# Performance work log

Measured on AMD Instinct MI355X. Metric: run time of the kernel, lower is better.

Reference implementation:

```python
import jax, jax.numpy as jnp
import numpy as np

EPS = 1e-5
TOP_K = 2


def setup_inputs() -> dict:
    key = jax.random.key(0)
    ks = jax.random.split(key, 6)
    T, H, F, E = 4096, 1024, 2816, 8
    scale = 0.02
    return {
        "hidden_states": jax.random.normal(ks[0], (T, H), dtype=jnp.float32),
        "ln_w": jnp.ones((H,), dtype=jnp.float32),
        "router_w": jax.random.normal(ks[1], (H, E), dtype=jnp.float32) * scale,
        "w_gate": jax.random.normal(ks[2], (E, H, F), dtype=jnp.float32) * scale,
        "w_up": jax.random.normal(ks[3], (E, H, F), dtype=jnp.float32) * scale,
        "w_down": jax.random.normal(ks[4], (E, F, H), dtype=jnp.float32) * scale,
    }


def reference(hidden_states, ln_w, router_w, w_gate, w_up, w_down):
    # RMSNorm (LlamaRMSNorm)
    var = jnp.mean(hidden_states * hidden_states, axis=-1, keepdims=True)
    x = hidden_states * jax.lax.rsqrt(var + EPS) * ln_w  # [T, H]

    # TopKRouter: softmax over experts, then top-k probs/indices
    logits = x @ router_w                     # [T, E]
    probs = jax.nn.softmax(logits, axis=-1)
    topk_p, topk_i = jax.lax.top_k(probs, TOP_K)  # [T, K]

    # Dense combine weights [T, E]: prob for routed experts, 0 otherwise
    T = x.shape[0]
    combine = jnp.zeros_like(probs).at[jnp.arange(T)[:, None], topk_i].add(topk_p)

    # Experts: Llama-style gated MLP (SwiGLU); loop over fixed small expert set
    out = jnp.zeros_like(x)
    for e in range(w_gate.shape[0]):
        h = jax.nn.silu(x @ w_gate[e]) * (x @ w_up[e])   # [T, F]
        out = out + combine[:, e:e + 1] * (h @ w_down[e])
    return out
```

## Files before the change

### kernel.cpp

```cpp
#include <hip/hip_runtime.h>

#define T_TOK 4096
#define H_DIM 1024
#define F_DIM 2816
#define E_NUM 8
#define EPSV 1e-5f

typedef unsigned short u16;
typedef __attribute__((ext_vector_type(8))) short bf16x8;
typedef __attribute__((ext_vector_type(4))) float f32x4;

__device__ __forceinline__ u16 f2bf(float f) {
  union { float f; unsigned u; } c; c.f = f;
  unsigned u = c.u;
  return (u16)((u + 0x7FFFu + ((u >> 16) & 1u)) >> 16);
}

__device__ __forceinline__ void llds16(const u16* g, u16* l) {
  __builtin_amdgcn_global_load_lds(
      (const __attribute__((address_space(1))) unsigned int*)g,
      (__attribute__((address_space(3))) unsigned int*)l, 16, 0, 0);
}

__global__ __launch_bounds__(256) void router_kernel(
    const float* __restrict__ hs, const float* __restrict__ lnw,
    const float* __restrict__ rw, u16* __restrict__ x_h,
    int* __restrict__ cnt, int* __restrict__ list,
    float* __restrict__ wcomb) {
  const int wave = threadIdx.x >> 6;
  const int lane = threadIdx.x & 63;
  const int t = blockIdx.x * 4 + wave;
  const float* row = hs + (size_t)t * H_DIM;

  float4 v[4];
  float ss = 0.f;
#pragma unroll
  for (int j = 0; j < 4; ++j) {
    v[j] = ((const float4*)row)[j * 64 + lane];
    ss += v[j].x * v[j].x + v[j].y * v[j].y + v[j].z * v[j].z + v[j].w * v[j].w;
  }
#pragma unroll
  for (int m = 32; m; m >>= 1) ss += __shfl_xor(ss, m, 64);
  const float inv = rsqrtf(ss * (1.0f / H_DIM) + EPSV);

  float lg[E_NUM];
#pragma unroll
  for (int e = 0; e < E_NUM; ++e) lg[e] = 0.f;

#pragma unroll
  for (int j = 0; j < 4; ++j) {
    const int idx = j * 64 + lane;
    const int h0 = idx * 4;
    float4 w4 = ((const float4*)lnw)[idx];
    float xv[4] = {v[j].x * inv * w4.x, v[j].y * inv * w4.y,
                   v[j].z * inv * w4.z, v[j].w * inv * w4.w};
    ushort4 xs;
    xs.x = f2bf(xv[0]); xs.y = f2bf(xv[1]); xs.z = f2bf(xv[2]); xs.w = f2bf(xv[3]);
    ((ushort4*)(x_h + (size_t)t * H_DIM))[idx] = xs;
#pragma unroll
    for (int q = 0; q < 4; ++q) {
      const float* rr = rw + (size_t)(h0 + q) * E_NUM;
      float4 a = ((const float4*)rr)[0];
      float4 b = ((const float4*)rr)[1];
      lg[0] += xv[q] * a.x; lg[1] += xv[q] * a.y;
      lg[2] += xv[q] * a.z; lg[3] += xv[q] * a.w;
      lg[4] += xv[q] * b.x; lg[5] += xv[q] * b.y;
      lg[6] += xv[q] * b.z; lg[7] += xv[q] * b.w;
    }
  }
#pragma unroll
  for (int e = 0; e < E_NUM; ++e)
#pragma unroll
    for (int m = 32; m; m >>= 1) lg[e] += __shfl_xor(lg[e], m, 64);

  if (lane == 0) {
    float mx = lg[0];
#pragma unroll
    for (int e = 1; e < E_NUM; ++e) mx = fmaxf(mx, lg[e]);
    float p[E_NUM], s = 0.f;
#pragma unroll
    for (int e = 0; e < E_NUM; ++e) { p[e] = __expf(lg[e] - mx); s += p[e]; }
    const float invs = 1.0f / s;
    int e1 = 0; float b1 = p[0];
#pragma unroll
    for (int e = 1; e < E_NUM; ++e) if (p[e] > b1) { b1 = p[e]; e1 = e; }
    int e2 = -1; float b2 = -1.f;
#pragma unroll
    for (int e = 0; e < E_NUM; ++e) if (e != e1 && p[e] > b2) { b2 = p[e]; e2 = e; }
    b1 *= invs; b2 *= invs;
    int p1 = atomicAdd(&cnt[e1], 1);
    list[e1 * T_TOK + p1] = t; wcomb[e1 * T_TOK + p1] = b1;
    int p2 = atomicAdd(&cnt[e2], 1);
    list[e2 * T_TOK + p2] = t; wcomb[e2 * T_TOK + p2] = b2;
  }
}

__global__ void offsets_kernel(const int* __restrict__ cnt, int* __restrict__ offs) {
  if (threadIdx.x == 0) {
    int s = 0;
    for (int e = 0; e < E_NUM; ++e) { offs[e] = s; s += cnt[e]; }
  }
}

#define TPW 5632
__global__ __launch_bounds__(256) void transpose_cvt_all(
    const float* __restrict__ wg, const float* __restrict__ wu,
    const float* __restrict__ wd, u16* __restrict__ wgT,
    u16* __restrict__ wuT, u16* __restrict__ wdT) {
  __shared__ float tile[128][37];
  const int bx = blockIdx.x;
  const int which = bx / TPW;
  const int rem = bx - which * TPW;
  const int e = rem / 704;
  const int t = rem - e * 704;
  const float* in; u16* outp; int R, C, rt, ct;
  if (which == 0)      { in = wg; outp = wgT; R = H_DIM; C = F_DIM; rt = t / 88; ct = t - rt * 88; }
  else if (which == 1) { in = wu; outp = wuT; R = H_DIM; C = F_DIM; rt = t / 88; ct = t - rt * 88; }
  else                 { in = wd; outp = wdT; R = F_DIM; C = H_DIM; rt = t >> 5; ct = t & 31; }
  const size_t base = (size_t)e * R * C;
  const int r0 = rt * 128, c0 = ct * 32;
  const int tid = threadIdx.x;

  const int rr = tid >> 3, cq = tid & 7;
#pragma unroll
  for (int i = 0; i < 4; ++i) {
    float4 v = *(const float4*)(in + base + (size_t)(r0 + rr + 32 * i) * C + c0 + cq * 4);
    float* dst = &tile[rr + 32 * i][cq * 4];
    dst[0] = v.x; dst[1] = v.y; dst[2] = v.z; dst[3] = v.w;
  }
  __syncthreads();

  const int cc = tid >> 4, rq0 = tid & 15;
#pragma unroll
  for (int jj = 0; jj < 4; ++jj) {
    const int c = cc + 16 * (jj & 1);
    const int rq = rq0 + 16 * (jj >> 1);
    ushort4 o;
    o.x = f2bf(tile[rq * 4 + 0][c]);
    o.y = f2bf(tile[rq * 4 + 1][c]);
    o.z = f2bf(tile[rq * 4 + 2][c]);
    o.w = f2bf(tile[rq * 4 + 3][c]);
    *(ushort4*)(outp + base + (size_t)(c0 + c) * R + r0 + rq * 4) = o;
  }
}

__global__ __launch_bounds__(256) void gemm1_kernel(
    const u16* __restrict__ x_h, const u16* __restrict__ wgT,
    const u16* __restrict__ wuT, const int* __restrict__ cnt,
    const int* __restrict__ offs, const int* __restrict__ list,
    u16* __restrict__ hbuf) {
  const int e = blockIdx.z;
  const int n_e = cnt[e];
  const int rt = blockIdx.y;
  if (rt * 128 >= n_e) return;
  const int ft = blockIdx.x;

  __shared__ __align__(16) u16 As[2][128 * 64];
  __shared__ __align__(16) u16 Bgs[2][64 * 64];
  __shared__ __align__(16) u16 Bus[2][64 * 64];

  const int tid = threadIdx.x;
  const int wv = tid >> 6, lane = tid & 63;
  const int wm = wv >> 1, wn = wv & 1;
  const int lrow = lane & 15, quad = lane >> 4;
  const int srow = lane >> 3, schunk = lane & 7;

  const u16* agp[4];
#pragma unroll
  for (int i = 0; i < 4; ++i) {
    const int rl = wv * 32 + i * 8 + srow;
    int gr = rt * 128 + rl; if (gr >= n_e) gr = n_e - 1;
    const int tkn = list[e * T_TOK + gr];
    agp[i] = x_h + (size_t)tkn * H_DIM + ((schunk ^ (rl & 7)) << 3);
  }
  const size_t wb = ((size_t)e * F_DIM + (size_t)ft * 64) * H_DIM;
  const u16* bgp[2]; const u16* bup[2];
#pragma unroll
  for (int i = 0; i < 2; ++i) {
    const int r = wv * 16 + i * 8 + srow;
    const size_t g = wb + (size_t)r * H_DIM + ((schunk ^ (r & 7)) << 3);
    bgp[i] = wgT + g;
    bup[i] = wuT + g;
  }

  int aoff[4][2], boff[2][2];
#pragma unroll
  for (int tm = 0; tm < 4; ++tm) {
    const int row = wm * 64 + tm * 16 + lrow;
#pragma unroll
    for (int ks = 0; ks < 2; ++ks)
      aoff[tm][ks] = row * 64 + (((ks * 4 + quad) ^ (row & 7)) << 3);
  }
#pragma unroll
  for (int tn = 0; tn < 2; ++tn) {
    const int row = wn * 32 + tn * 16 + lrow;
#pragma unroll
    for (int ks = 0; ks < 2; ++ks)
      boff[tn][ks] = row * 64 + (((ks * 4 + quad) ^ (row & 7)) << 3);
  }

  f32x4 accg[4][2], accu[4][2];
#pragma unroll
  for (int i = 0; i < 4; ++i)
#pragma unroll
    for (int j = 0; j < 2; ++j) {
      accg[i][j] = f32x4{0.f, 0.f, 0.f, 0.f};
      accu[i][j] = f32x4{0.f, 0.f, 0.f, 0.f};
    }

  auto stage = [&](int b, int k0) {
#pragma unroll
    for (int i = 0; i < 4; ++i)
      llds16(agp[i] + k0, &As[b][(wv * 32 + i * 8) * 64]);
#pragma unroll
    for (int i = 0; i < 2; ++i) {
      llds16(bgp[i] + k0, &Bgs[b][(wv * 16 + i * 8) * 64]);
      llds16(bup[i] + k0, &Bus[b][(wv * 16 + i * 8) * 64]);
    }
  };
  auto compute = [&](int b) {
#pragma unroll
    for (int ks = 0; ks < 2; ++ks) {
      bf16x8 a[4], bg[2], bu[2];
#pragma unroll
      for (int tm = 0; tm < 4; ++tm) a[tm] = *(const bf16x8*)&As[b][aoff[tm][ks]];
#pragma unroll
      for (int tn = 0; tn < 2; ++tn) {
        bg[tn] = *(const bf16x8*)&Bgs[b][boff[tn][ks]];
        bu[tn] = *(const bf16x8*)&Bus[b][boff[tn][ks]];
      }
#pragma unroll
      for (int tm = 0; tm < 4; ++tm)
#pragma unroll
        for (int tn = 0; tn < 2; ++tn) {
          accg[tm][tn] = __builtin_amdgcn_mfma_f32_16x16x32_bf16(a[tm], bg[tn], accg[tm][tn], 0, 0, 0);
          accu[tm][tn] = __builtin_amdgcn_mfma_f32_16x16x32_bf16(a[tm], bu[tn], accu[tm][tn], 0, 0, 0);
        }
    }
  };

  stage(0, 0);
#pragma unroll 1
  for (int k0 = 0; k0 < H_DIM; k0 += 128) {
    const bool s1 = (k0 + 64) < H_DIM;
    if (s1) {
      stage(1, k0 + 64);
      asm volatile("s_waitcnt vmcnt(8)" ::: "memory");
    } else {
      asm volatile("s_waitcnt vmcnt(0)" ::: "memory");
    }
    __builtin_amdgcn_s_barrier();
    compute(0);
    __builtin_amdgcn_s_barrier();
    const bool s2 = (k0 + 128) < H_DIM;
    if (s2) {
      stage(0, k0 + 128);
      asm volatile("s_waitcnt vmcnt(8)" ::: "memory");
    } else {
      asm volatile("s_waitcnt vmcnt(0)" ::: "memory");
    }
    __builtin_amdgcn_s_barrier();
    compute(1);
    __builtin_amdgcn_s_barrier();
  }

  const int oe = offs[e];
#pragma unroll
  for (int tm = 0; tm < 4; ++tm) {
    const int lr0 = wm * 64 + tm * 16 + quad * 4;
#pragma unroll
    for (int rr = 0; rr < 4; ++rr) {
      const int gr = rt * 128 + lr0 + rr;
      if (gr < n_e) {
#pragma unroll
        for (int tn = 0; tn < 2; ++tn) {
          float g = accg[tm][tn][rr];
          float u = accu[tm][tn][rr];
          float hv = g / (1.0f + __expf(-g)) * u;
          int col = ft * 64 + wn * 32 + tn * 16 + lrow;
          hbuf[(size_t)(oe + gr) * F_DIM + col] = f2bf(hv);
        }
      }
    }
  }
}

__global__ __launch_bounds__(256) void gemm2_kernel(
    const u16* __restrict__ hbuf, const u16* __restrict__ wdT,
    const int* __restrict__ cnt, const int* __restrict__ offs,
    const float* __restrict__ wcomb, const int* __restrict__ list,
    float* __restrict__ out) {
  const int e = blockIdx.z;
  const int n_e = cnt[e];
  const int rt = blockIdx.y;
  if (rt * 128 >= n_e) return;
  const int nt = blockIdx.x;

  __shared__ __align__(16) u16 As[2][128 * 64];
  __shared__ __align__(16) u16 Bs[2][128 * 64];

  const int tid = threadIdx.x;
  const int oe = offs[e];
  const int wv = tid >> 6, lane = tid & 63;
  const int wm = wv >> 1, wn = wv & 1;
  const int lrow = lane & 15, quad = lane >> 4;
  const int srow = lane >> 3, schunk = lane & 7;

  const u16* agp[4];
#pragma unroll
  for (int i = 0; i < 4; ++i) {
    const int rl = wv * 32 + i * 8 + srow;
    int gr = rt * 128 + rl; if (gr >= n_e) gr = n_e - 1;
    agp[i] = hbuf + (size_t)(oe + gr) * F_DIM + ((schunk ^ (rl & 7)) << 3);
  }
  const size_t wb = ((size_t)e * H_DIM + (size_t)nt * 128) * F_DIM;
  const u16* bgp[4];
#pragma unroll
  for (int i = 0; i < 4; ++i) {
    const int r = wv * 32 + i * 8 + srow;
    bgp[i] = wdT + wb + (size_t)r * F_DIM + ((schunk ^ (r & 7)) << 3);
  }

  int aoff[4][2], boff[4][2];
#pragma unroll
  for (int tm = 0; tm < 4; ++tm) {
    const int row = wm * 64 + tm * 16 + lrow;
#pragma unroll
    for (int ks = 0; ks < 2; ++ks)
      aoff[tm][ks] = row * 64 + (((ks * 4 + quad) ^ (row & 7)) << 3);
  }
#pragma unroll
  for (int tn = 0; tn < 4; ++tn) {
    const int row = wn * 64 + tn * 16 + lrow;
#pragma unroll
    for (int ks = 0; ks < 2; ++ks)
      boff[tn][ks] = row * 64 + (((ks * 4 + quad) ^ (row & 7)) << 3);
  }

  f32x4 acc[4][4];
#pragma unroll
  for (int i = 0; i < 4; ++i)
#pragma unroll
    for (int j = 0; j < 4; ++j) acc[i][j] = f32x4{0.f, 0.f, 0.f, 0.f};

  auto stage = [&](int b, int k0) {
#pragma unroll
    for (int i = 0; i < 4; ++i) {
      llds16(agp[i] + k0, &As[b][(wv * 32 + i * 8) * 64]);
      llds16(bgp[i] + k0, &Bs[b][(wv * 32 + i * 8) * 64]);
    }
  };
  auto compute = [&](int b) {
#pragma unroll
    for (int ks = 0; ks < 2; ++ks) {
      bf16x8 a[4], bb[4];
#pragma unroll
      for (int tm = 0; tm < 4; ++tm) a[tm] = *(const bf16x8*)&As[b][aoff[tm][ks]];
#pragma unroll
      for (int tn = 0; tn < 4; ++tn) bb[tn] = *(const bf16x8*)&Bs[b][boff[tn][ks]];
#pragma unroll
      for (int tm = 0; tm < 4; ++tm)
#pragma unroll
        for (int tn = 0; tn < 4; ++tn)
          acc[tm][tn] = __builtin_amdgcn_mfma_f32_16x16x32_bf16(a[tm], bb[tn], acc[tm][tn], 0, 0, 0);
    }
  };

  stage(0, 0);
#pragma unroll 1
  for (int k0 = 0; k0 < F_DIM; k0 += 128) {
    const bool s1 = (k0 + 64) < F_DIM;
    if (s1) {
      stage(1, k0 + 64);
      asm volatile("s_waitcnt vmcnt(8)" ::: "memory");
    } else {
      asm volatile("s_waitcnt vmcnt(0)" ::: "memory");
    }
    __builtin_amdgcn_s_barrier();
    compute(0);
    __builtin_amdgcn_s_barrier();
    const bool s2 = (k0 + 128) < F_DIM;
    if (s2) {
      stage(0, k0 + 128);
      asm volatile("s_waitcnt vmcnt(8)" ::: "memory");
    } else {
      asm volatile("s_waitcnt vmcnt(0)" ::: "memory");
    }
    __builtin_amdgcn_s_barrier();
    compute(1);
    __builtin_amdgcn_s_barrier();
  }

#pragma unroll
  for (int tm = 0; tm < 4; ++tm) {
    const int lr0 = wm * 64 + tm * 16 + quad * 4;
#pragma unroll
    for (int rr = 0; rr < 4; ++rr) {
      const int gr = rt * 128 + lr0 + rr;
      if (gr < n_e) {
        const float cw = wcomb[e * T_TOK + gr];
        const int tkn = list[e * T_TOK + gr];
#pragma unroll
        for (int tn = 0; tn < 4; ++tn) {
          const int col = nt * 128 + wn * 64 + tn * 16 + lrow;
          atomicAdd(&out[(size_t)tkn * H_DIM + col], acc[tm][tn][rr] * cw);
        }
      }
    }
  }
}

extern "C" void kernel_launch(void* const* d_in, const int* in_sizes, int n_in,
                              void* d_out, int out_size, void* d_ws, size_t ws_size,
                              hipStream_t stream) {
  const float* hs  = (const float*)d_in[0];
  const float* lnw = (const float*)d_in[1];
  const float* rw  = (const float*)d_in[2];
  const float* wg  = (const float*)d_in[3];
  const float* wu  = (const float*)d_in[4];
  const float* wd  = (const float*)d_in[5];
  float* out = (float*)d_out;

  char* p = (char*)d_ws;
  const size_t SZ_XH = (size_t)T_TOK * H_DIM * 2;
  const size_t SZ_W  = (size_t)E_NUM * F_DIM * H_DIM * 2;
  const size_t SZ_HB = (size_t)T_TOK * 2 * F_DIM * 2;

  u16* x_h  = (u16*)p;   p += SZ_XH;
  u16* wgT  = (u16*)p;   p += SZ_W;
  u16* wuT  = (u16*)p;   p += SZ_W;
  u16* wdT  = (u16*)p;   p += SZ_W;
  u16* hbuf = (u16*)p;   p += SZ_HB;
  int* cnt  = (int*)p;   p += 256;
  int* offs = (int*)p;   p += 256;
  int* list = (int*)p;   p += (size_t)E_NUM * T_TOK * 4;
  float* wcomb = (float*)p; p += (size_t)E_NUM * T_TOK * 4;

  hipMemsetAsync(cnt, 0, 256, stream);
  hipMemsetAsync(out, 0, (size_t)T_TOK * H_DIM * 4, stream);
  router_kernel<<<T_TOK / 4, 256, 0, stream>>>(hs, lnw, rw, x_h, cnt, list, wcomb);
  offsets_kernel<<<1, 64, 0, stream>>>(cnt, offs);
  transpose_cvt_all<<<3 * TPW, 256, 0, stream>>>(wg, wu, wd, wgT, wuT, wdT);
  gemm1_kernel<<<dim3(F_DIM / 64, T_TOK / 128, E_NUM), 256, 0, stream>>>(x_h, wgT, wuT, cnt, offs, list, hbuf);
  gemm2_kernel<<<dim3(H_DIM / 128, T_TOK / 128, E_NUM), 256, 0, stream>>>(hbuf, wdT, cnt, offs, wcomb, list, out);
}
```

Measured before the change: 669.3 us.

## Compact expert tile map, single-buffer GEMMs for occupancy, replace atomics with combine

Adds a compacted tile map so both GEMMs launch only over real (expert, row-tile) pairs instead of a sparse 3D grid full of early-exit blocks. Drops the LDS double buffering in both GEMMs and adds launch bounds requesting 4 blocks per CU, trading software prefetch for more resident waves. The atomicAdd scatter into the output is replaced by dense per-slot writes and a separate combine kernel that sums each token's two expert rows. This removes the output memset, but adds a 32 MB intermediate buffer and an extra kernel launch.

```diff
diff --git a/kernel.cpp b/kernel.cpp
--- a/kernel.cpp
+++ b/kernel.cpp
@@ -5,6 +5,7 @@
 #define F_DIM 2816
 #define E_NUM 8
 #define EPSV 1e-5f
+#define MAX_TILES 72
 
 typedef unsigned short u16;
 typedef __attribute__((ext_vector_type(8))) short bf16x8;
@@ -26,7 +27,7 @@
     const float* __restrict__ hs, const float* __restrict__ lnw,
     const float* __restrict__ rw, u16* __restrict__ x_h,
     int* __restrict__ cnt, int* __restrict__ list,
-    float* __restrict__ wcomb) {
+    float* __restrict__ wcomb, int* __restrict__ slot) {
   const int wave = threadIdx.x >> 6;
   const int lane = threadIdx.x & 63;
   const int t = blockIdx.x * 4 + wave;
@@ -90,15 +91,23 @@
     b1 *= invs; b2 *= invs;
     int p1 = atomicAdd(&cnt[e1], 1);
     list[e1 * T_TOK + p1] = t; wcomb[e1 * T_TOK + p1] = b1;
+    slot[2 * t] = (e1 << 16) | p1;
     int p2 = atomicAdd(&cnt[e2], 1);
     list[e2 * T_TOK + p2] = t; wcomb[e2 * T_TOK + p2] = b2;
-  }
-}
-
-__global__ void offsets_kernel(const int* __restrict__ cnt, int* __restrict__ offs) {
+    slot[2 * t + 1] = (e2 << 16) | p2;
+  }
+}
+
+__global__ void offsets_kernel(const int* __restrict__ cnt, int* __restrict__ offs,
+                               int* __restrict__ tmap) {
   if (threadIdx.x == 0) {
-    int s = 0;
-    for (int e = 0; e < E_NUM; ++e) { offs[e] = s; s += cnt[e]; }
+    int s = 0, ty = 0;
+    for (int e = 0; e < E_NUM; ++e) {
+      offs[e] = s; s += cnt[e];
+      const int nt = (cnt[e] + 127) >> 7;
+      for (int r = 0; r < nt; ++r) tmap[ty++] = (e << 16) | r;
+    }
+    for (; ty < MAX_TILES; ++ty) tmap[ty] = -1;
   }
 }
 
@@ -144,20 +153,20 @@
   }
 }
 
-__global__ __launch_bounds__(256) void gemm1_kernel(
+__global__ __launch_bounds__(256, 4) void gemm1_kernel(
     const u16* __restrict__ x_h, const u16* __restrict__ wgT,
     const u16* __restrict__ wuT, const int* __restrict__ cnt,
     const int* __restrict__ offs, const int* __restrict__ list,
-    u16* __restrict__ hbuf) {
-  const int e = blockIdx.z;
+    const int* __restrict__ tmap, u16* __restrict__ hbuf) {
+  const int tme = tmap[blockIdx.y];
+  if (tme < 0) return;
+  const int e = tme >> 16, rt = tme & 0xFFFF;
   const int n_e = cnt[e];
-  const int rt = blockIdx.y;
-  if (rt * 128 >= n_e) return;
   const int ft = blockIdx.x;
 
-  __shared__ __align__(16) u16 As[2][128 * 64];
-  __shared__ __align__(16) u16 Bgs[2][64 * 64];
-  __shared__ __align__(16) u16 Bus[2][64 * 64];
+  __shared__ __align__(16) u16 As[128 * 64];
+  __shared__ __align__(16) u16 Bgs[64 * 64];
+  __shared__ __align__(16) u16 Bus[64 * 64];
 
   const int tid = threadIdx.x;
   const int wv = tid >> 6, lane = tid & 63;
@@ -208,26 +217,26 @@
       accu[i][j] = f32x4{0.f, 0.f, 0.f, 0.f};
     }
 
-  auto stage = [&](int b, int k0) {
+#pragma unroll 1
+  for (int k0 = 0; k0 < H_DIM; k0 += 64) {
 #pragma unroll
     for (int i = 0; i < 4; ++i)
-      llds16(agp[i] + k0, &As[b][(wv * 32 + i * 8) * 64]);
+      llds16(agp[i] + k0, &As[(wv * 32 + i * 8) * 64]);
 #pragma unroll
     for (int i = 0; i < 2; ++i) {
-      llds16(bgp[i] + k0, &Bgs[b][(wv * 16 + i * 8) * 64]);
-      llds16(bup[i] + k0, &Bus[b][(wv * 16 + i * 8) * 64]);
-    }
-  };
-  auto compute = [&](int b) {
+      llds16(bgp[i] + k0, &Bgs[(wv * 16 + i * 8) * 64]);
+      llds16(bup[i] + k0, &Bus[(wv * 16 + i * 8) * 64]);
+    }
+    __syncthreads();
 #pragma unroll
     for (int ks = 0; ks < 2; ++ks) {
       bf16x8 a[4], bg[2], bu[2];
 #pragma unroll
-      for (int tm = 0; tm < 4; ++tm) a[tm] = *(const bf16x8*)&As[b][aoff[tm][ks]];
+      for (int tm = 0; tm < 4; ++tm) a[tm] = *(const bf16x8*)&As[aoff[tm][ks]];
 #pragma unroll
       for (int tn = 0; tn < 2; ++tn) {
-        bg[tn] = *(const bf16x8*)&Bgs[b][boff[tn][ks]];
-        bu[tn] = *(const bf16x8*)&Bus[b][boff[tn][ks]];
+        bg[tn] = *(const bf16x8*)&Bgs[boff[tn][ks]];
+        bu[tn] = *(const bf16x8*)&Bus[boff[tn][ks]];
       }
 #pragma unroll
       for (int tm = 0; tm < 4; ++tm)
@@ -237,31 +246,7 @@
           accu[tm][tn] = __builtin_amdgcn_mfma_f32_16x16x32_bf16(a[tm], bu[tn], accu[tm][tn], 0, 0, 0);
         }
     }
-  };
-
-  stage(0, 0);
-#pragma unroll 1
-  for (int k0 = 0; k0 < H_DIM; k0 += 128) {
-    const bool s1 = (k0 + 64) < H_DIM;
-    if (s1) {
-      stage(1, k0 + 64);
-      asm volatile("s_waitcnt vmcnt(8)" ::: "memory");
-    } else {
-      asm volatile("s_waitcnt vmcnt(0)" ::: "memory");
-    }
-    __builtin_amdgcn_s_barrier();
-    compute(0);
-    __builtin_amdgcn_s_barrier();
-    const bool s2 = (k0 + 128) < H_DIM;
-    if (s2) {
-      stage(0, k0 + 128);
-      asm volatile("s_waitcnt vmcnt(8)" ::: "memory");
-    } else {
-      asm volatile("s_waitcnt vmcnt(0)" ::: "memory");
-    }
-    __builtin_amdgcn_s_barrier();
-    compute(1);
-    __builtin_amdgcn_s_barrier();
+    __syncthreads();
   }
 
   const int oe = offs[e];
@@ -285,19 +270,19 @@
   }
 }
 
-__global__ __launch_bounds__(256) void gemm2_kernel(
+__global__ __launch_bounds__(256, 4) void gemm2_kernel(
     const u16* __restrict__ hbuf, const u16* __restrict__ wdT,
     const int* __restrict__ cnt, const int* __restrict__ offs,
-    const float* __restrict__ wcomb, const int* __restrict__ list,
-    float* __restrict__ out) {
-  const int e = blockIdx.z;
+    const float* __restrict__ wcomb, const int* __restrict__ tmap,
+    float* __restrict__ contrib) {
+  const int tme = tmap[blockIdx.y];
+  if (tme < 0) return;
+  const int e = tme >> 16, rt = tme & 0xFFFF;
   const int n_e = cnt[e];
-  const int rt = blockIdx.y;
-  if (rt * 128 >= n_e) return;
   const int nt = blockIdx.x;
 
-  __shared__ __align__(16) u16 As[2][128 * 64];
-  __shared__ __align__(16) u16 Bs[2][128 * 64];
+  __shared__ __align__(16) u16 As[128 * 64];
+  __shared__ __align__(16) u16 Bs[128 * 64];
 
   const int tid = threadIdx.x;
   const int oe = offs[e];
@@ -343,52 +328,28 @@
 #pragma unroll
     for (int j = 0; j < 4; ++j) acc[i][j] = f32x4{0.f, 0.f, 0.f, 0.f};
 
-  auto stage = [&](int b, int k0) {
+#pragma unroll 1
+  for (int k0 = 0; k0 < F_DIM; k0 += 64) {
 #pragma unroll
     for (int i = 0; i < 4; ++i) {
-      llds16(agp[i] + k0, &As[b][(wv * 32 + i * 8) * 64]);
-      llds16(bgp[i] + k0, &Bs[b][(wv * 32 + i * 8) * 64]);
-    }
-  };
-  auto compute = [&](int b) {
+      llds16(agp[i] + k0, &As[(wv * 32 + i * 8) * 64]);
+      llds16(bgp[i] + k0, &Bs[(wv * 32 + i * 8) * 64]);
+    }
+    __syncthreads();
 #pragma unroll
     for (int ks = 0; ks < 2; ++ks) {
       bf16x8 a[4], bb[4];
 #pragma unroll
-      for (int tm = 0; tm < 4; ++tm) a[tm] = *(const bf16x8*)&As[b][aoff[tm][ks]];
-#pragma unroll
-      for (int tn = 0; tn < 4; ++tn) bb[tn] = *(const bf16x8*)&Bs[b][boff[tn][ks]];
+      for (int tm = 0; tm < 4; ++tm) a[tm] = *(const bf16x8*)&As[aoff[tm][ks]];
+#pragma unroll
+      for (int tn = 0; tn < 4; ++tn) bb[tn] = *(const bf16x8*)&Bs[boff[tn][ks]];
 #pragma unroll
       for (int tm = 0; tm < 4; ++tm)
 #pragma unroll
         for (int tn = 0; tn < 4; ++tn)
           acc[tm][tn] = __builtin_amdgcn_mfma_f32_16x16x32_bf16(a[tm], bb[tn], acc[tm][tn], 0, 0, 0);
     }
-  };
-
-  stage(0, 0);
-#pragma unroll 1
-  for (int k0 = 0; k0 < F_DIM; k0 += 128) {
-    const bool s1 = (k0 + 64) < F_DIM;
-    if (s1) {
-      stage(1, k0 + 64);
-      asm volatile("s_waitcnt vmcnt(8)" ::: "memory");
-    } else {
-      asm volatile("s_waitcnt vmcnt(0)" ::: "memory");
-    }
-    __builtin_amdgcn_s_barrier();
-    compute(0);
-    __builtin_amdgcn_s_barrier();
-    const bool s2 = (k0 + 128) < F_DIM;
-    if (s2) {
-      stage(0, k0 + 128);
-      asm volatile("s_waitcnt vmcnt(8)" ::: "memory");
-    } else {
-      asm volatile("s_waitcnt vmcnt(0)" ::: "memory");
-    }
-    __builtin_amdgcn_s_barrier();
-    compute(1);
-    __builtin_amdgcn_s_barrier();
+    __syncthreads();
   }
 
 #pragma unroll
@@ -399,15 +360,27 @@
       const int gr = rt * 128 + lr0 + rr;
       if (gr < n_e) {
         const float cw = wcomb[e * T_TOK + gr];
-        const int tkn = list[e * T_TOK + gr];
 #pragma unroll
         for (int tn = 0; tn < 4; ++tn) {
           const int col = nt * 128 + wn * 64 + tn * 16 + lrow;
-          atomicAdd(&out[(size_t)tkn * H_DIM + col], acc[tm][tn][rr] * cw);
+          contrib[(size_t)(oe + gr) * H_DIM + col] = acc[tm][tn][rr] * cw;
         }
       }
     }
   }
+}
+
+__global__ __launch_bounds__(256) void combine_kernel(
+    const float* __restrict__ contrib, const int* __restrict__ offs,
+    const int* __restrict__ slot, float* __restrict__ out) {
+  const int t = blockIdx.x;
+  const int s0 = slot[2 * t], s1 = slot[2 * t + 1];
+  const int r0 = offs[s0 >> 16] + (s0 & 0xFFFF);
+  const int r1 = offs[s1 >> 16] + (s1 & 0xFFFF);
+  float4 a = ((const float4*)(contrib + (size_t)r0 * H_DIM))[threadIdx.x];
+  float4 b = ((const float4*)(contrib + (size_t)r1 * H_DIM))[threadIdx.x];
+  float4 o = {a.x + b.x, a.y + b.y, a.z + b.z, a.w + b.w};
+  ((float4*)(out + (size_t)t * H_DIM))[threadIdx.x] = o;
 }
 
 extern "C" void kernel_launch(void* const* d_in, const int* in_sizes, int n_in,
@@ -425,22 +398,26 @@
   const size_t SZ_XH = (size_t)T_TOK * H_DIM * 2;
   const size_t SZ_W  = (size_t)E_NUM * F_DIM * H_DIM * 2;
   const size_t SZ_HB = (size_t)T_TOK * 2 * F_DIM * 2;
+  const size_t SZ_CT = (size_t)T_TOK * 2 * H_DIM * 4;
 
   u16* x_h  = (u16*)p;   p += SZ_XH;
   u16* wgT  = (u16*)p;   p += SZ_W;
   u16* wuT  = (u16*)p;   p += SZ_W;
   u16* wdT  = (u16*)p;   p += SZ_W;
   u16* hbuf = (u16*)p;   p += SZ_HB;
+  float* contrib = (float*)p; p += SZ_CT;
   int* cnt  = (int*)p;   p += 256;
   int* offs = (int*)p;   p += 256;
+  int* tmap = (int*)p;   p += 512;
   int* list = (int*)p;   p += (size_t)E_NUM * T_TOK * 4;
   float* wcomb = (float*)p; p += (size_t)E_NUM * T_TOK * 4;
+  int* slot = (int*)p;   p += (size_t)T_TOK * 2 * 4;
 
   hipMemsetAsync(cnt, 0, 256, stream);
-  hipMemsetAsync(out, 0, (size_t)T_TOK * H_DIM * 4, stream);
-  router_kernel<<<T_TOK / 4, 256, 0, stream>>>(hs, lnw, rw, x_h, cnt, list, wcomb);
-  offsets_kernel<<<1, 64, 0, stream>>>(cnt, offs);
+  router_kernel<<<T_TOK / 4, 256, 0, stream>>>(hs, lnw, rw, x_h, cnt, list, wcomb, slot);
+  offsets_kernel<<<1, 64, 0, stream>>>(cnt, offs, tmap);
   transpose_cvt_all<<<3 * TPW, 256, 0, stream>>>(wg, wu, wd, wgT, wuT, wdT);
-  gemm1_kernel<<<dim3(F_DIM / 64, T_TOK / 128, E_NUM), 256, 0, stream>>>(x_h, wgT, wuT, cnt, offs, list, hbuf);
-  gemm2_kernel<<<dim3(H_DIM / 128, T_TOK / 128, E_NUM), 256, 0, stream>>>(hbuf, wdT, cnt, offs, wcomb, list, out);
-}
+  gemm1_kernel<<<dim3(F_DIM / 64, MAX_TILES), 256, 0, stream>>>(x_h, wgT, wuT, cnt, offs, list, tmap, hbuf);
+  gemm2_kernel<<<dim3(H_DIM / 128, MAX_TILES), 256, 0, stream>>>(hbuf, wdT, cnt, offs, wcomb, tmap, contrib);
+  combine_kernel<<<T_TOK, 256, 0, stream>>>(contrib, offs, slot, out);
+}
```

Measured after the change: 588.1 us. -12.1%, faster.
